# Kernel tuning notes

Hardware: AMD Instinct MI355X
Metric: run time of the kernel (lower is better)

Reference implementation:

```python
import math
import jax, jax.numpy as jnp
import numpy as np

DIM = 512
HEADS = 8
HEAD_DIM = DIM // HEADS


def get_slopes(n):
    def pow2(n):
        start = 2 ** (-2 ** (-(math.log2(n) - 3)))
        return [start * start ** i for i in range(n)]
    if math.log2(n).is_integer():
        return pow2(n)
    c = 2 ** math.floor(math.log2(n))
    return pow2(c) + get_slopes(2 * c)[0::2][: n - c]


def setup_inputs() -> dict:
    key = jax.random.key(0)
    ks = jax.random.split(key, 12)
    b, n, d = 2, 4096, DIM
    s = 1.0 / math.sqrt(d)
    inp = {
        "x": jax.random.normal(ks[0], (b, n, d), jnp.float32),
        # coords in a ~[0,100) spatial range (tile grid coordinates)
        "coords": jax.random.uniform(ks[1], (b, n, 2), jnp.float32) * 100.0,
        "Wq": jax.random.normal(ks[2], (d, d), jnp.float32) * s,
        "bq": jnp.zeros((d,), jnp.float32),
        "Wk": jax.random.normal(ks[3], (d, d), jnp.float32) * s,
        "bk": jnp.zeros((d,), jnp.float32),
        "Wv": jax.random.normal(ks[4], (d, d), jnp.float32) * s,
        "bv": jnp.zeros((d,), jnp.float32),
        "Wp": jax.random.normal(ks[5], (d, d), jnp.float32) * s,
        "bp": jnp.zeros((d,), jnp.float32),
        "slopes": jnp.asarray(get_slopes(HEADS), jnp.float32),  # [h]
    }
    return inp


def reference(x, coords, Wq, bq, Wk, bk, Wv, bv, Wp, bp, slopes):
    b, n_q, d = x.shape
    h, hd = HEADS, HEAD_DIM
    # self-attention: context = x, context_coords = coords
    q = (x @ Wq + bq).reshape(b, n_q, h, hd).transpose(0, 2, 1, 3)  # b h nq hd
    k = (x @ Wk + bk).reshape(b, n_q, h, hd).transpose(0, 2, 1, 3)
    v = (x @ Wv + bv).reshape(b, n_q, h, hd).transpose(0, 2, 1, 3)
    # Euclidean-distance ALiBi bias: [b, h, nq, nk]
    diff = coords[:, :, None, :] - coords[:, None, :, :]          # b nq nk 2
    dist = jnp.sqrt(jnp.sum(diff * diff, axis=-1))                # b nq nk
    bias = -slopes[None, :, None, None] * dist[:, None, :, :]     # b h nq nk
    scores = jnp.einsum("bhqd,bhkd->bhqk", q, k) / math.sqrt(hd) + bias
    attn = jax.nn.softmax(scores, axis=-1)
    out = jnp.einsum("bhqk,bhkd->bhqd", attn, v)
    out = out.transpose(0, 2, 1, 3).reshape(b, n_q, d)
    return out @ Wp + bp
```

## Files before the change

### kernel.cpp

```cpp
#include <hip/hip_runtime.h>
#include <stdint.h>

typedef __bf16 bf16;
typedef __attribute__((ext_vector_type(8))) __bf16 bf16x8;
typedef __attribute__((ext_vector_type(4))) __bf16 bf16x4;
typedef __attribute__((ext_vector_type(4))) float f32x4;

#define DEVFN static __device__ __forceinline__

DEVFN void gload16(const bf16* g, char* l) {
  __builtin_amdgcn_global_load_lds(
      (const __attribute__((address_space(1))) void*)g,
      (__attribute__((address_space(3))) void*)l, 16, 0, 0);
}
DEVFN void gload4(const float* g, char* l) {
  __builtin_amdgcn_global_load_lds(
      (const __attribute__((address_space(1))) void*)g,
      (__attribute__((address_space(3))) void*)l, 4, 0, 0);
}

DEVFN int swz(int row, int kb) { return row * 128 + (kb ^ ((row & 7) << 4)); }

__global__ __launch_bounds__(256) void prep_kernel(
    const float* __restrict__ x, const float* __restrict__ Wq,
    const float* __restrict__ Wk, const float* __restrict__ Wv,
    const float* __restrict__ Wp, bf16* __restrict__ xb,
    bf16* __restrict__ Wt, bf16* __restrict__ Wpt) {
  const int64_t tid = blockIdx.x * 256LL + threadIdx.x;
  const int64_t stride = (int64_t)gridDim.x * 256LL;
  for (int64_t i = tid; i < (8192LL * 512) / 4; i += stride) {
    float4 v = ((const float4*)x)[i];
    bf16x4 o = {(bf16)v.x, (bf16)v.y, (bf16)v.z, (bf16)v.w};
    ((bf16x4*)xb)[i] = o;
  }
  for (int64_t i = tid; i < 1536LL * 512; i += stride) {
    int c = (int)(i >> 9), k = (int)(i & 511);
    int wsel = c >> 9, cc = c & 511;
    const float* W = wsel == 0 ? Wq : (wsel == 1 ? Wk : Wv);
    Wt[i] = (bf16)W[k * 512 + cc];
  }
  for (int64_t i = tid; i < 512LL * 512; i += stride) {
    int c = (int)(i >> 9), k = (int)(i & 511);
    Wpt[i] = (bf16)Wp[k * 512 + c];
  }
}

DEVFN void gemm_main(const bf16* __restrict__ A, const bf16* __restrict__ B,
                     int rowA0, int rowB0, char* sA, char* sB, f32x4 acc[4][4],
                     int wr, int wc, int lane, int w) {
#pragma unroll
  for (int m = 0; m < 4; m++)
#pragma unroll
    for (int n = 0; n < 4; n++) acc[m][n] = (f32x4){0.f, 0.f, 0.f, 0.f};
  const int lr = lane >> 3;
  const int kswz = 8 * ((lane & 7) ^ lr);
  for (int k0 = 0; k0 < 512; k0 += 64) {
#pragma unroll
    for (int j = 0; j < 4; j++) {
      const int c = w * 4 + j;
      gload16(A + (rowA0 + c * 8 + lr) * 512 + k0 + kswz, sA + c * 1024);
      gload16(B + (rowB0 + c * 8 + lr) * 512 + k0 + kswz, sB + c * 1024);
    }
    __syncthreads();
    bf16x8 af[4][2], bfv[4][2];
#pragma unroll
    for (int m = 0; m < 4; m++)
#pragma unroll
      for (int kk = 0; kk < 2; kk++) {
        af[m][kk] = *(const bf16x8*)(sA + swz(wr * 64 + m * 16 + (lane & 15),
                                              kk * 64 + (lane >> 4) * 16));
        bfv[m][kk] = *(const bf16x8*)(sB + swz(wc * 64 + m * 16 + (lane & 15),
                                               kk * 64 + (lane >> 4) * 16));
      }
#pragma unroll
    for (int m = 0; m < 4; m++)
#pragma unroll
      for (int n = 0; n < 4; n++)
#pragma unroll
        for (int kk = 0; kk < 2; kk++)
          acc[m][n] = __builtin_amdgcn_mfma_f32_16x16x32_bf16(
              af[m][kk], bfv[n][kk], acc[m][n], 0, 0, 0);
    __syncthreads();
  }
}

__global__ __launch_bounds__(256) void qkv_gemm(
    const bf16* __restrict__ xb, const bf16* __restrict__ Wt,
    const float* __restrict__ bq, const float* __restrict__ bk,
    const float* __restrict__ bv, bf16* __restrict__ Qb, bf16* __restrict__ Kb,
    bf16* __restrict__ Vt) {
  __shared__ __align__(128) char sA[16384];
  __shared__ __align__(128) char sB[16384];
  const int lane = threadIdx.x & 63, w = threadIdx.x >> 6;
  const int wr = w >> 1, wc = w & 1;
  const int rowA0 = blockIdx.y * 128;
  const int colB0 = blockIdx.x * 128;
  f32x4 acc[4][4];
  gemm_main(xb, Wt, rowA0, colB0, sA, sB, acc, wr, wc, lane, w);
  const int which = colB0 >> 9;
  const int cc0 = colB0 & 511;
  const float* bias = which == 0 ? bq : (which == 1 ? bk : bv);
  const float QSCALE = 0.18033688011112042f;
#pragma unroll
  for (int m = 0; m < 4; m++)
#pragma unroll
    for (int n = 0; n < 4; n++)
#pragma unroll
      for (int r = 0; r < 4; r++) {
        int row = rowA0 + wr * 64 + m * 16 + (lane >> 4) * 4 + r;
        int col = cc0 + wc * 64 + n * 16 + (lane & 15);
        float v = acc[m][n][r] + bias[col];
        if (which == 0) {
          Qb[(int64_t)row * 512 + col] = (bf16)(v * QSCALE);
        } else if (which == 1) {
          Kb[(int64_t)row * 512 + col] = (bf16)v;
        } else {
          int b = row >> 12, nn = row & 4095;
          int hh = col >> 6, e = col & 63;
          Vt[(((int64_t)(b * 8 + hh)) * 64 + e) * 4096 + nn] = (bf16)v;
        }
      }
}

__global__ __launch_bounds__(256) void out_gemm(const bf16* __restrict__ Ob,
                                                const bf16* __restrict__ Wpt,
                                                const float* __restrict__ bp,
                                                float* __restrict__ out) {
  __shared__ __align__(128) char sA[16384];
  __shared__ __align__(128) char sB[16384];
  const int lane = threadIdx.x & 63, w = threadIdx.x >> 6;
  const int wr = w >> 1, wc = w & 1;
  const int rowA0 = blockIdx.y * 128;
  const int colB0 = blockIdx.x * 128;
  f32x4 acc[4][4];
  gemm_main(Ob, Wpt, rowA0, colB0, sA, sB, acc, wr, wc, lane, w);
#pragma unroll
  for (int m = 0; m < 4; m++)
#pragma unroll
    for (int n = 0; n < 4; n++)
#pragma unroll
      for (int r = 0; r < 4; r++) {
        int row = rowA0 + wr * 64 + m * 16 + (lane >> 4) * 4 + r;
        int col = colB0 + wc * 64 + n * 16 + (lane & 15);
        out[(int64_t)row * 512 + col] = acc[m][n][r] + bp[col];
      }
}

__global__ __launch_bounds__(512) void attn_kernel(
    const bf16* __restrict__ Qb, const bf16* __restrict__ Kb,
    const bf16* __restrict__ Vt, const float* __restrict__ coords,
    const float* __restrict__ slopes, bf16* __restrict__ Ob) {
  __shared__ __align__(128) char sK[2 * 8192];
  __shared__ __align__(128) char sV[2 * 10240];
  __shared__ __align__(128) char sC[2 * 256];
  __shared__ __align__(128) char sP[8 * 1280];

  const int tid = threadIdx.x;
  const int lane = tid & 63, w = tid >> 6;
  const int c = lane & 15, g = lane >> 4;

  const int id = blockIdx.x;
  const int combo = id & 7;
  const int qt = id >> 3;
  const int b = combo >> 2, hp = combo & 3;
  const int q0 = qt * 64;
  const int qsub = w >> 1;
  const int hl = w & 1;
  const int h = hp * 2 + hl;
  const int qw = q0 + qsub * 16;
  const int bO = b * 4096;

  const float LOG2E = 1.4426950408889634f;
  const float negsl2 = -slopes[h] * LOG2E;

  bf16x8 aq[2];
  {
    int64_t base = ((int64_t)(bO + qw + c)) * 512 + h * 64 + g * 8;
    aq[0] = *(const bf16x8*)(Qb + base);
    aq[1] = *(const bf16x8*)(Qb + base + 32);
  }
  const float* cbf = coords + (int64_t)bO * 2;
  float qcx, qcy;
  {
    float2 qc = ((const float2*)cbf)[qw + c];
    qcx = qc.x;
    qcy = qc.y;
  }

  bf16x8 ones;
#pragma unroll
  for (int jj = 0; jj < 8; jj++) ones[jj] = (bf16)1.0f;

  float m2 = -1e30f;
  f32x4 o[4], osum;
#pragma unroll
  for (int n = 0; n < 4; n++) o[n] = (f32x4){0.f, 0.f, 0.f, 0.f};
  osum = (f32x4){0.f, 0.f, 0.f, 0.f};

  const bf16* Vbase = Vt + (int64_t)(b * 8 + hp * 2) * 64 * 4096;

  const int krr = w * 4 + (lane >> 4);
  const int kgs = (lane & 15) ^ (krr & 7);
  auto vstage = [&](int j, int kv0, char* dstb) {
    const int hj = j >= 5 ? 1 : 0;
    const int cj = j - hj * 5;
    const int G = cj * 64 + lane;
    const int row = (G * 52429) >> 18;
    int gr = G - row * 5;
    if (gr > 3) gr = 0;
    gload16(Vbase + (int64_t)hj * 262144 + row * 4096 + kv0 + gr * 8,
            dstb + hj * 5120 + cj * 1024);
  };
  auto STAGE = [&](int tile, int bb) {
    const int kv0 = tile * 32;
    gload16(Kb + (int64_t)(bO + kv0 + krr) * 512 + hp * 128 + kgs * 8,
            sK + bb * 8192 + w * 1024);
    vstage(w, kv0, sV + bb * 10240);
    if (w < 2) vstage(8 + w, kv0, sV + bb * 10240);
    if (w == 7) gload4(cbf + kv0 * 2 + lane, sC + bb * 256);
  };

  STAGE(0, 0);
  __syncthreads();

  char* pwv = sP + w * 1280;
  for (int tt = 0; tt < 128; ++tt) {
    const int bb = tt & 1;
    if (tt + 1 < 128) STAGE(tt + 1, bb ^ 1);

    const char* kb = sK + bb * 8192;
    const char* vb = sV + bb * 10240 + hl * 5120;
    const char* cbuf = sC + bb * 256;

    bf16x8 kf[2][2];
#pragma unroll
    for (int t = 0; t < 2; t++)
#pragma unroll
      for (int kk = 0; kk < 2; kk++) {
        const int row = t * 16 + c;
        const int pg = (hl * 8 + kk * 4 + g) ^ (c & 7);
        kf[t][kk] = *(const bf16x8*)(kb + row * 256 + pg * 16);
      }
    float s[2][4];
    __builtin_amdgcn_s_setprio(1);
#pragma unroll
    for (int t = 0; t < 2; t++) {
      f32x4 sa = (f32x4){0.f, 0.f, 0.f, 0.f};
      sa = __builtin_amdgcn_mfma_f32_16x16x32_bf16(kf[t][0], aq[0], sa, 0, 0, 0);
      sa = __builtin_amdgcn_mfma_f32_16x16x32_bf16(kf[t][1], aq[1], sa, 0, 0, 0);
#pragma unroll
      for (int r = 0; r < 4; r++) s[t][r] = sa[r];
    }
    __builtin_amdgcn_s_setprio(0);

#pragma unroll
    for (int t = 0; t < 2; t++) {
      f32x4 ca = *(const f32x4*)(cbuf + 128 * t + 32 * g);
      f32x4 cb = *(const f32x4*)(cbuf + 128 * t + 32 * g + 16);
      float dx, dy;
#define DIST1(T, R, CX, CY)                                              \
  dx = qcx - (CX);                                                       \
  dy = qcy - (CY);                                                       \
  s[T][R] = __builtin_fmaf(__builtin_amdgcn_sqrtf(dx * dx + dy * dy),    \
                           negsl2, s[T][R]);
      DIST1(t, 0, ca[0], ca[1])
      DIST1(t, 1, ca[2], ca[3])
      DIST1(t, 2, cb[0], cb[1])
      DIST1(t, 3, cb[2], cb[3])
#undef DIST1
    }

    float lm = fmaxf(fmaxf(fmaxf(s[0][0], s[0][1]), fmaxf(s[0][2], s[0][3])),
                     fmaxf(fmaxf(s[1][0], s[1][1]), fmaxf(s[1][2], s[1][3])));
    lm = fmaxf(lm, __shfl_xor(lm, 16));
    lm = fmaxf(lm, __shfl_xor(lm, 32));
    if (__any(lm > m2 + 8.f)) {
      float nm = fmaxf(m2, lm);
      float sc = __builtin_amdgcn_exp2f(m2 - nm);
      m2 = nm;
      float scr[4];
#pragma unroll
      for (int r = 0; r < 4; r++)
        scr[r] = __shfl(sc, (lane & 48) | (4 * g + r));
#pragma unroll
      for (int n = 0; n < 4; n++)
#pragma unroll
        for (int r = 0; r < 4; r++) o[n][r] *= scr[r];
#pragma unroll
      for (int r = 0; r < 4; r++) osum[r] *= scr[r];
    }

#pragma unroll
    for (int t = 0; t < 2; t++) {
      bf16x4 pv = {(bf16)__builtin_amdgcn_exp2f(s[t][0] - m2),
                   (bf16)__builtin_amdgcn_exp2f(s[t][1] - m2),
                   (bf16)__builtin_amdgcn_exp2f(s[t][2] - m2),
                   (bf16)__builtin_amdgcn_exp2f(s[t][3] - m2)};
      const int L = 2 * t + (g >> 1);
      *(bf16x4*)(pwv + c * 80 + L * 16 + (g & 1) * 8) = pv;
    }
    bf16x8 pa = *(const bf16x8*)(pwv + c * 80 + g * 16);

    __builtin_amdgcn_s_setprio(1);
#pragma unroll
    for (int n = 0; n < 4; n++) {
      bf16x8 vf = *(const bf16x8*)(vb + (n * 16 + c) * 80 + g * 16);
      o[n] = __builtin_amdgcn_mfma_f32_16x16x32_bf16(pa, vf, o[n], 0, 0, 0);
    }
    osum = __builtin_amdgcn_mfma_f32_16x16x32_bf16(pa, ones, osum, 0, 0, 0);
    __builtin_amdgcn_s_setprio(0);

    __syncthreads();
  }

#pragma unroll
  for (int r = 0; r < 4; r++) {
    float inv = 1.f / osum[r];
    int64_t row = (int64_t)bO + qw + g * 4 + r;
#pragma unroll
    for (int n = 0; n < 4; n++)
      Ob[row * 512 + h * 64 + n * 16 + c] = (bf16)(o[n][r] * inv);
  }
}

extern "C" void kernel_launch(void* const* d_in, const int* in_sizes, int n_in,
                              void* d_out, int out_size, void* d_ws,
                              size_t ws_size, hipStream_t stream) {
  const float* x = (const float*)d_in[0];
  const float* coords = (const float*)d_in[1];
  const float* Wq = (const float*)d_in[2];
  const float* bq = (const float*)d_in[3];
  const float* Wk = (const float*)d_in[4];
  const float* bk = (const float*)d_in[5];
  const float* Wv = (const float*)d_in[6];
  const float* bv = (const float*)d_in[7];
  const float* Wp = (const float*)d_in[8];
  const float* bp = (const float*)d_in[9];
  const float* slopes = (const float*)d_in[10];

  char* ws = (char*)d_ws;
  bf16* xb = (bf16*)(ws);
  bf16* Wt = (bf16*)(ws + 8388608);
  bf16* Wpt = (bf16*)(ws + 9961472);
  bf16* Qb = (bf16*)(ws + 10485760);
  bf16* Kb = (bf16*)(ws + 18874368);
  bf16* Vt = (bf16*)(ws + 27262976);
  bf16* Ob = (bf16*)(ws + 35651584);

  hipLaunchKernelGGL(prep_kernel, dim3(1024), dim3(256), 0, stream, x, Wq, Wk,
                     Wv, Wp, xb, Wt, Wpt);
  hipLaunchKernelGGL(qkv_gemm, dim3(12, 64), dim3(256), 0, stream, xb, Wt, bq,
                     bk, bv, Qb, Kb, Vt);
  hipLaunchKernelGGL(attn_kernel, dim3(512), dim3(512), 0, stream, Qb, Kb,
                     Vt, coords, slopes, Ob);
  hipLaunchKernelGGL(out_gemm, dim3(4, 64), dim3(256), 0, stream, Ob, Wpt, bp,
                     (float*)d_out);
}
```

Before: 236.0 us.

## Split attention KV range in two with partial outputs and a combine kernel

The attention kernel now processes one head per block with 128 queries, and splits the 4096-key range into two halves across blocks (split-K / flash-decoding style), giving 1024 blocks instead of 512. Each block writes its running max, row sum and unnormalized bf16 output to a partials buffer, and a new combine kernel merges the two halves with log-sum-exp rescaling. This raises parallelism and halves the per-block shared-memory staging. In exchange it adds an extra kernel launch, a workspace round-trip for the partials, and an extra bf16 rounding of the unnormalized outputs.

```diff
diff --git a/kernel.cpp b/kernel.cpp
--- a/kernel.cpp
+++ b/kernel.cpp
@@ -20,6 +20,8 @@
 }
 
 DEVFN int swz(int row, int kb) { return row * 128 + (kb ^ ((row & 7) << 4)); }
+
+#define PS 9437184LL
 
 __global__ __launch_bounds__(256) void prep_kernel(
     const float* __restrict__ x, const float* __restrict__ Wq,
@@ -149,9 +151,9 @@
 __global__ __launch_bounds__(512) void attn_kernel(
     const bf16* __restrict__ Qb, const bf16* __restrict__ Kb,
     const bf16* __restrict__ Vt, const float* __restrict__ coords,
-    const float* __restrict__ slopes, bf16* __restrict__ Ob) {
-  __shared__ __align__(128) char sK[2 * 8192];
-  __shared__ __align__(128) char sV[2 * 10240];
+    const float* __restrict__ slopes, char* __restrict__ part) {
+  __shared__ __align__(128) char sK[2 * 4096];
+  __shared__ __align__(128) char sV[2 * 5120];
   __shared__ __align__(128) char sC[2 * 256];
   __shared__ __align__(128) char sP[8 * 1280];
 
@@ -160,15 +162,13 @@
   const int c = lane & 15, g = lane >> 4;
 
   const int id = blockIdx.x;
-  const int combo = id & 7;
-  const int qt = id >> 3;
-  const int b = combo >> 2, hp = combo & 3;
-  const int q0 = qt * 64;
-  const int qsub = w >> 1;
-  const int hl = w & 1;
-  const int h = hp * 2 + hl;
-  const int qw = q0 + qsub * 16;
+  const int bh = id & 15;
+  const int qt = (id >> 4) & 31;
+  const int ks = id >> 9;
+  const int b = bh >> 3, h = bh & 7;
+  const int qw = qt * 128 + w * 16;
   const int bO = b * 4096;
+  const int kvs = ks * 2048;
 
   const float LOG2E = 1.4426950408889634f;
   const float negsl2 = -slopes[h] * LOG2E;
@@ -197,50 +197,48 @@
   for (int n = 0; n < 4; n++) o[n] = (f32x4){0.f, 0.f, 0.f, 0.f};
   osum = (f32x4){0.f, 0.f, 0.f, 0.f};
 
-  const bf16* Vbase = Vt + (int64_t)(b * 8 + hp * 2) * 64 * 4096;
-
-  const int krr = w * 4 + (lane >> 4);
-  const int kgs = (lane & 15) ^ (krr & 7);
-  auto vstage = [&](int j, int kv0, char* dstb) {
-    const int hj = j >= 5 ? 1 : 0;
-    const int cj = j - hj * 5;
-    const int G = cj * 64 + lane;
+  const bf16* Kp = Kb + (int64_t)bO * 512 + h * 64;
+  const bf16* Vp = Vt + (int64_t)(b * 8 + h) * 262144;
+
+  auto vstage = [&](int j, int kv0, int bb) {
+    const int G = j * 64 + lane;
     const int row = (G * 52429) >> 18;
     int gr = G - row * 5;
     if (gr > 3) gr = 0;
-    gload16(Vbase + (int64_t)hj * 262144 + row * 4096 + kv0 + gr * 8,
-            dstb + hj * 5120 + cj * 1024);
+    gload16(Vp + row * 4096 + kv0 + gr * 8, sV + bb * 5120 + j * 1024);
   };
   auto STAGE = [&](int tile, int bb) {
-    const int kv0 = tile * 32;
-    gload16(Kb + (int64_t)(bO + kv0 + krr) * 512 + hp * 128 + kgs * 8,
-            sK + bb * 8192 + w * 1024);
-    vstage(w, kv0, sV + bb * 10240);
-    if (w < 2) vstage(8 + w, kv0, sV + bb * 10240);
-    if (w == 7) gload4(cbf + kv0 * 2 + lane, sC + bb * 256);
+    const int kv0 = kvs + tile * 32;
+    if (w < 4) {
+      gload16(Kp + (int64_t)(kv0 + w * 8 + (lane >> 3)) * 512 +
+                  ((lane & 7) ^ ((lane >> 3) & 7)) * 8,
+              sK + bb * 4096 + w * 1024);
+    } else {
+      vstage(w - 4, kv0, bb);
+    }
+    if (w == 0) vstage(4, kv0, bb);
+    if (w == 1) gload4(cbf + kv0 * 2 + lane, sC + bb * 256);
   };
 
   STAGE(0, 0);
   __syncthreads();
 
   char* pwv = sP + w * 1280;
-  for (int tt = 0; tt < 128; ++tt) {
+  for (int tt = 0; tt < 64; ++tt) {
     const int bb = tt & 1;
-    if (tt + 1 < 128) STAGE(tt + 1, bb ^ 1);
-
-    const char* kb = sK + bb * 8192;
-    const char* vb = sV + bb * 10240 + hl * 5120;
+    if (tt + 1 < 64) STAGE(tt + 1, bb ^ 1);
+
+    const char* kb = sK + bb * 4096;
+    const char* vb = sV + bb * 5120;
     const char* cbuf = sC + bb * 256;
 
     bf16x8 kf[2][2];
 #pragma unroll
     for (int t = 0; t < 2; t++)
 #pragma unroll
-      for (int kk = 0; kk < 2; kk++) {
-        const int row = t * 16 + c;
-        const int pg = (hl * 8 + kk * 4 + g) ^ (c & 7);
-        kf[t][kk] = *(const bf16x8*)(kb + row * 256 + pg * 16);
-      }
+      for (int kk = 0; kk < 2; kk++)
+        kf[t][kk] = *(const bf16x8*)(kb + (t * 16 + c) * 128 +
+                                     (((kk * 4 + g) ^ (c & 7)) * 16));
     float s[2][4];
     __builtin_amdgcn_s_setprio(1);
 #pragma unroll
@@ -256,7 +254,7 @@
 #pragma unroll
     for (int t = 0; t < 2; t++) {
       f32x4 ca = *(const f32x4*)(cbuf + 128 * t + 32 * g);
-      f32x4 cb = *(const f32x4*)(cbuf + 128 * t + 32 * g + 16);
+      f32x4 cb2 = *(const f32x4*)(cbuf + 128 * t + 32 * g + 16);
       float dx, dy;
 #define DIST1(T, R, CX, CY)                                              \
   dx = qcx - (CX);                                                       \
@@ -265,8 +263,8 @@
                            negsl2, s[T][R]);
       DIST1(t, 0, ca[0], ca[1])
       DIST1(t, 1, ca[2], ca[3])
-      DIST1(t, 2, cb[0], cb[1])
-      DIST1(t, 3, cb[2], cb[3])
+      DIST1(t, 2, cb2[0], cb2[1])
+      DIST1(t, 3, cb2[2], cb2[3])
 #undef DIST1
     }
 
@@ -313,14 +311,41 @@
     __syncthreads();
   }
 
+  float m2r[4];
+#pragma unroll
+  for (int r = 0; r < 4; r++)
+    m2r[r] = __shfl(m2, (lane & 48) | (4 * g + r));
+  char* pb0 = part + ks * PS + ((int64_t)bh * 4096 + qw) * 144;
 #pragma unroll
   for (int r = 0; r < 4; r++) {
-    float inv = 1.f / osum[r];
-    int64_t row = (int64_t)bO + qw + g * 4 + r;
+    char* pb = pb0 + (g * 4 + r) * 144;
+    if (c == 0) {
+      *(float*)pb = m2r[r];
+      *((float*)pb + 1) = osum[r];
+    }
 #pragma unroll
     for (int n = 0; n < 4; n++)
-      Ob[row * 512 + h * 64 + n * 16 + c] = (bf16)(o[n][r] * inv);
-  }
+      *(bf16*)(pb + 16 + (n * 16 + c) * 2) = (bf16)o[n][r];
+  }
+}
+
+__global__ __launch_bounds__(256) void combine_kernel(
+    const char* __restrict__ part, bf16* __restrict__ Ob) {
+  const int t = blockIdx.x * 256 + threadIdx.x;
+  const int row = t >> 6;
+  const int e = t & 63;
+  const char* p0 = part + (int64_t)row * 144;
+  const char* p1 = p0 + PS;
+  const float m0 = *(const float*)p0, s0 = *((const float*)p0 + 1);
+  const float m1 = *(const float*)p1, s1 = *((const float*)p1 + 1);
+  const float o0 = (float)*(const bf16*)(p0 + 16 + e * 2);
+  const float o1 = (float)*(const bf16*)(p1 + 16 + e * 2);
+  const float m = fmaxf(m0, m1);
+  const float w0 = __builtin_amdgcn_exp2f(m0 - m);
+  const float w1 = __builtin_amdgcn_exp2f(m1 - m);
+  const float res = (o0 * w0 + o1 * w1) / (s0 * w0 + s1 * w1);
+  const int bh = row >> 12, q = row & 4095;
+  Ob[((int64_t)((bh >> 3) * 4096 + q)) * 512 + (bh & 7) * 64 + e] = (bf16)res;
 }
 
 extern "C" void kernel_launch(void* const* d_in, const int* in_sizes, int n_in,
@@ -346,13 +371,16 @@
   bf16* Kb = (bf16*)(ws + 18874368);
   bf16* Vt = (bf16*)(ws + 27262976);
   bf16* Ob = (bf16*)(ws + 35651584);
+  char* part = ws + 44040192;
 
   hipLaunchKernelGGL(prep_kernel, dim3(1024), dim3(256), 0, stream, x, Wq, Wk,
                      Wv, Wp, xb, Wt, Wpt);
   hipLaunchKernelGGL(qkv_gemm, dim3(12, 64), dim3(256), 0, stream, xb, Wt, bq,
                      bk, bv, Qb, Kb, Vt);
-  hipLaunchKernelGGL(attn_kernel, dim3(512), dim3(512), 0, stream, Qb, Kb,
-                     Vt, coords, slopes, Ob);
+  hipLaunchKernelGGL(attn_kernel, dim3(1024), dim3(512), 0, stream, Qb, Kb,
+                     Vt, coords, slopes, part);
+  hipLaunchKernelGGL(combine_kernel, dim3(16384), dim3(256), 0, stream, part,
+                     Ob);
   hipLaunchKernelGGL(out_gemm, dim3(4, 64), dim3(256), 0, stream, Ob, Wpt, bp,
                      (float*)d_out);
 }
```

Measured after the change: 232.6 us. No clear change (-1.4%).
